# Optimization experiments

Hardware: AMD Instinct MI355X
Metric: run time of the kernel (lower is better)

Reference implementation:

```python
import jax, jax.numpy as jnp
import numpy as np

B, L, E, H = 4, 2048, 1024, 16
HD = E // H  # 64
ROPE_BASE = 10000.0


def setup_inputs() -> dict:
    key = jax.random.key(0)
    ks = jax.random.split(key, 4)
    x = jax.random.normal(ks[0], (B, L, E), dtype=jnp.float32)
    Wqkv = jax.random.normal(ks[1], (3 * E, E), dtype=jnp.float32) * (E ** -0.5)
    bqkv = jnp.zeros((3 * E,), dtype=jnp.float32)
    Wout = jax.random.normal(ks[2], (E, E), dtype=jnp.float32) * (E ** -0.5)
    bout = jnp.zeros((E,), dtype=jnp.float32)
    # RoPE tables: (1, 1, L, HD/2)
    half = HD // 2
    inv_freq = 1.0 / (ROPE_BASE ** (jnp.arange(half, dtype=jnp.float32) / half))
    t = jnp.arange(L, dtype=jnp.float32)
    freqs = t[:, None] * inv_freq[None, :]  # (L, half)
    cos = jnp.cos(freqs)[None, None]
    sin = jnp.sin(freqs)[None, None]
    return {"x": x, "cos": cos, "sin": sin, "Wqkv": Wqkv, "bqkv": bqkv,
            "Wout": Wout, "bout": bout}


def _apply_rope(q, k, cos, sin):
    half = q.shape[-1] // 2
    q1, q2 = q[..., :half], q[..., half:]
    k1, k2 = k[..., :half], k[..., half:]
    q_rot = jnp.concatenate([q1 * cos - q2 * sin, q1 * sin + q2 * cos], axis=-1)
    k_rot = jnp.concatenate([k1 * cos - k2 * sin, k1 * sin + k2 * cos], axis=-1)
    return q_rot, k_rot


def reference(x, cos, sin, Wqkv, bqkv, Wout, bout):
    b, l, e = x.shape
    qkv = x @ Wqkv.T + bqkv  # (B, L, 3E)
    q, k, v = jnp.split(qkv, 3, axis=-1)
    # (B, H, L, HD)
    q = q.reshape(b, l, H, HD).transpose(0, 2, 1, 3)
    k = k.reshape(b, l, H, HD).transpose(0, 2, 1, 3)
    v = v.reshape(b, l, H, HD).transpose(0, 2, 1, 3)
    q, k = _apply_rope(q, k, cos, sin)
    scale = 1.0 / jnp.sqrt(jnp.asarray(HD, dtype=x.dtype))
    scores = jnp.einsum('bhqd,bhkd->bhqk', q, k) * scale
    attn = jax.nn.softmax(scores, axis=-1)
    out = jnp.einsum('bhqk,bhkd->bhqd', attn, v)  # (B, H, L, HD)
    out = out.transpose(0, 2, 1, 3).reshape(b, l, e)
    out = out @ Wout.T + bout
    return out
```

## Files before the change

### kernel.cpp

```cpp
#include <hip/hip_runtime.h>
#include <math.h>

#define B 4
#define L 2048
#define E 1024
#define H 16
#define HD 64
#define MROWS (B*L)
#define E3 (3*E)

using bf16x8   = __attribute__((ext_vector_type(8))) short;
using f16x8    = __attribute__((ext_vector_type(8))) _Float16;
using floatx4  = __attribute__((ext_vector_type(4))) float;
using floatx16 = __attribute__((ext_vector_type(16))) float;

__device__ inline ushort f2bf(float x) {
    uint u = __float_as_uint(x);
    u += 0x7FFF + ((u >> 16) & 1);
    return (ushort)(u >> 16);
}
__device__ inline float bf2f(ushort h) { return __uint_as_float(((uint)h) << 16); }
__device__ inline ushort f2h(float x) { _Float16 h = (_Float16)x; return *(ushort*)&h; }

#if __has_builtin(__builtin_amdgcn_exp2f)
#define EXP2F(x) __builtin_amdgcn_exp2f(x)
#else
#define EXP2F(x) exp2f(x)
#endif

__device__ inline void async16(const void* g, void* l) {
    __builtin_amdgcn_global_load_lds(
        (const __attribute__((address_space(1))) uint*)g,
        (__attribute__((address_space(3))) uint*)l, 16, 0, 0);
}

__device__ inline uint pack_rtz(float odd, float even) {
    return __builtin_amdgcn_perm(__float_as_uint(odd), __float_as_uint(even), 0x07060302u);
}

#define N1Q ((size_t)MROWS * E / 4)
#define N2Q ((size_t)E3 * E / 4)
#define N3Q ((size_t)E * E / 4)
__global__ __launch_bounds__(256) void cvt_all(
        const float* __restrict__ x, const float* __restrict__ wq,
        const float* __restrict__ wo, ushort* __restrict__ x16,
        ushort* __restrict__ wq16, ushort* __restrict__ wo16)
{
    size_t i = (size_t)blockIdx.x * 256 + threadIdx.x;
    const float* src; ushort* dst; size_t j;
    if (i < N1Q)                  { src = x;  dst = x16;  j = i; }
    else if (i < N1Q + N2Q)       { src = wq; dst = wq16; j = i - N1Q; }
    else                          { src = wo; dst = wo16; j = i - N1Q - N2Q; }
    float4 v = ((const float4*)src)[j];
    ushort4 o;
    o.x = f2h(v.x); o.y = f2h(v.y); o.z = f2h(v.z); o.w = f2h(v.w);
    ((ushort4*)dst)[j] = o;
}

template<int MODE>
__global__ __launch_bounds__(256) void gemm_f16(
        const ushort* __restrict__ A16, const ushort* __restrict__ B16,
        const float* __restrict__ bias, float* __restrict__ Cf,
        ushort* __restrict__ qh, ushort* __restrict__ kh, ushort* __restrict__ vT,
        const float* __restrict__ cosT, const float* __restrict__ sinT,
        int Ndim, int Kdim)
{
    __shared__ ushort lds[2][8192];

    const int tid = threadIdx.x;
    const int w = tid >> 6, lane = tid & 63;
    const int g = lane >> 4, c = lane & 15;
    const int m0 = blockIdx.y * 128, n0 = blockIdx.x * 128;
    const int wm = w & 1, wn = w >> 1;

    const int rl0 = lane >> 2;
    const int jsw = (lane & 3) ^ ((lane >> 3) & 3);
    const ushort* gbase = (w < 2) ? A16 + (size_t)(m0 + 64 * (w & 1)) * Kdim
                                  : B16 + (size_t)(n0 + 64 * (w & 1)) * Kdim;
    const ushort* lanesrc = gbase + (size_t)rl0 * Kdim + jsw * 8;
    const int ldoff = (w >> 1) * 4096 + (w & 1) * 2048;

    floatx4 acc[4][4];
#pragma unroll
    for (int a = 0; a < 4; ++a)
#pragma unroll
        for (int bq = 0; bq < 4; ++bq) acc[a][bq] = (floatx4){0.f, 0.f, 0.f, 0.f};

    const int swz  = (g ^ ((c >> 1) & 3)) * 8;
    const int arow = wm * 2048 + c * 32;
    const int brow = 4096 + wn * 2048 + c * 32;

#pragma unroll
    for (int p = 0; p < 4; ++p)
        async16(lanesrc + (size_t)p * 16 * Kdim, &lds[0][ldoff + p * 512]);

    const int NK = Kdim >> 5;
    for (int kk = 0; kk < NK; ++kk) {
        const int pb = kk & 1;
        __syncthreads();

        if (kk + 1 < NK) {
            const ushort* ns = lanesrc + (size_t)(kk + 1) * 32;
#pragma unroll
            for (int p = 0; p < 4; ++p)
                async16(ns + (size_t)p * 16 * Kdim, &lds[pb ^ 1][ldoff + p * 512]);
        }

        const ushort* cur = &lds[pb][0];
        f16x8 af[4], bf[4];
#pragma unroll
        for (int t = 0; t < 4; ++t) {
            af[t] = *(const f16x8*)&cur[arow + t * 512 + swz];
            bf[t] = *(const f16x8*)&cur[brow + t * 512 + swz];
        }
#pragma unroll
        for (int mt = 0; mt < 4; ++mt)
#pragma unroll
            for (int nt = 0; nt < 4; ++nt)
                acc[mt][nt] = __builtin_amdgcn_mfma_f32_16x16x32_f16(af[mt], bf[nt], acc[mt][nt], 0, 0, 0);
    }

    const int colbase = n0 + wn * 64;
#pragma unroll
    for (int mt = 0; mt < 4; ++mt) {
        const int rowb = m0 + wm * 64 + mt * 16 + g * 4;
        if constexpr (MODE == 2) {
#pragma unroll
            for (int i = 0; i < 4; ++i) {
                const int row = rowb + i;
#pragma unroll
                for (int nt = 0; nt < 4; ++nt) {
                    const int col = colbase + nt * 16 + c;
                    Cf[(size_t)row * Ndim + col] = acc[mt][nt][i] + bias[col];
                }
            }
        } else {
            const int sec = colbase >> 10;
            const int hg  = (colbase & 1023) >> 6;
#pragma unroll
            for (int i = 0; i < 4; ++i) {
                const int row = rowb + i;
                const int bb = row >> 11;
                const int l  = row & (L - 1);
                if (sec < 2) {
                    ushort* dst = (sec == 0 ? qh : kh) + ((size_t)(bb * H + hg) * L + l) * HD;
                    const int sw = l & 7;
                    const float qs = (sec == 0) ? 0.18033688f : 1.0f;
#pragma unroll
                    for (int nt = 0; nt < 2; ++nt) {
                        const int d  = nt * 16 + c;
                        const int d2 = d + 32;
                        float v1 = acc[mt][nt][i]     + bias[colbase + d];
                        float v2 = acc[mt][nt + 2][i] + bias[colbase + d2];
                        float cs = cosT[l * 32 + d], sn = sinT[l * 32 + d];
                        dst[(((d  >> 3) ^ sw) << 3) | (d  & 7)] = f2bf((v1 * cs - v2 * sn) * qs);
                        dst[(((d2 >> 3) ^ sw) << 3) | (d2 & 7)] = f2bf((v1 * sn + v2 * cs) * qs);
                    }
                } else {
                    const int lp = (l & ~12) | ((l & 4) << 1) | ((l & 8) >> 1);
                    const int intile = ((((lp >> 3) & 7)) << 3);
#pragma unroll
                    for (int nt = 0; nt < 4; ++nt) {
                        const int d = nt * 16 + c;
                        float v = acc[mt][nt][i] + bias[colbase + d];
                        size_t idx = ((size_t)(bb * H + hg) * HD + d) * L
                                   + (l & ~63) + (intile ^ ((d & 7) << 3)) + (lp & 7);
                        vT[idx] = f2bf(v);
                    }
                }
            }
        }
    }
}

__global__ __launch_bounds__(256, 4) void flash_mfma4(
        const ushort* __restrict__ qh, const ushort* __restrict__ kh,
        const ushort* __restrict__ vT, ushort* __restrict__ attn16)
{
    __shared__ ushort Ks[2][4096];
    __shared__ ushort Vt[2][4096];

    const int tid  = threadIdx.x;
    const int w    = tid >> 6;
    const int lane = tid & 63;
    const int h    = lane >> 5;
    const int n    = lane & 31;
    const int b    = blockIdx.x >> 4;
    const int hd   = blockIdx.x & 15;
    const int q0   = blockIdx.y * 128;

    const ushort* khead = kh + (size_t)(b * H + hd) * L * HD;
    const ushort* vhead = vT + (size_t)(b * H + hd) * HD * L;

    const int q = q0 + 32 * w + n;
    const ushort* qrow = qh + ((size_t)(b * H + hd) * L + q) * HD;
    bf16x8 aq[4];
#pragma unroll
    for (int kd = 0; kd < 4; ++kd)
        aq[kd] = *(const bf16x8*)&qrow[((2 * kd + h) ^ (q & 7)) << 3];

    const int wk = w & 1;
    const ushort* ksrc = khead + (size_t)(32 * wk) * 64 + lane * 8;
    const ushort* vsrc = vhead + (size_t)(32 * wk + (lane >> 3)) * L + (lane & 7) * 8;

    const int NIT = L / 64;
    if (w < 2) {
#pragma unroll
        for (int p = 0; p < 4; ++p)
            async16(ksrc + p * 512, &Ks[0][32 * wk * 64 + p * 512]);
    } else {
#pragma unroll
        for (int p = 0; p < 4; ++p)
            async16(vsrc + (size_t)p * 8 * L, &Vt[0][32 * wk * 64 + p * 512]);
    }

    float l_i = 0.f;
    floatx16 o[2];
    o[0] = (floatx16)(0.f);
    o[1] = (floatx16)(0.f);

    for (int it = 0; it < NIT; ++it) {
        const int p = it & 1;
        __syncthreads();

        if (it + 1 < NIT) {
            if (w < 2) {
                const ushort* s = ksrc + (size_t)(it + 1) * 4096;
#pragma unroll
                for (int pp = 0; pp < 4; ++pp)
                    async16(s + pp * 512, &Ks[p ^ 1][32 * wk * 64 + pp * 512]);
            } else {
                const ushort* s = vsrc + (size_t)(it + 1) * 64;
#pragma unroll
                for (int pp = 0; pp < 4; ++pp)
                    async16(s + (size_t)pp * 8 * L, &Vt[p ^ 1][32 * wk * 64 + pp * 512]);
            }
        }

        const ushort* KsC = Ks[p];
        const ushort* VtC = Vt[p];

#pragma unroll
        for (int js = 0; js < 2; ++js) {
            floatx16 s = (floatx16)(-16.0f);
#pragma unroll
            for (int kd = 0; kd < 4; ++kd) {
                bf16x8 kf = *(const bf16x8*)&KsC[(32 * js + n) * 64 + (((2 * kd + h) ^ (n & 7)) << 3)];
                s = __builtin_amdgcn_mfma_f32_32x32x16_bf16(kf, aq[kd], s, 0, 0, 0);
            }

            float pv[16];
            float rs = 0.f;
#pragma unroll
            for (int rr = 0; rr < 4; ++rr) {
                float p0 = EXP2F(s[4 * rr + 0]);
                float p1 = EXP2F(s[4 * rr + 1]);
                float p2 = EXP2F(s[4 * rr + 2]);
                float p3 = EXP2F(s[4 * rr + 3]);
                pv[4 * rr + 0] = p0; pv[4 * rr + 1] = p1;
                pv[4 * rr + 2] = p2; pv[4 * rr + 3] = p3;
                rs += (p0 + p1) + (p2 + p3);
            }
            l_i += rs;

#pragma unroll
            for (int f = 0; f < 2; ++f) {
                uint bu[4];
                bu[0] = pack_rtz(pv[8 * f + 1], pv[8 * f + 0]);
                bu[1] = pack_rtz(pv[8 * f + 3], pv[8 * f + 2]);
                bu[2] = pack_rtz(pv[8 * f + 5], pv[8 * f + 4]);
                bu[3] = pack_rtz(pv[8 * f + 7], pv[8 * f + 6]);
                bf16x8 bp = *(const bf16x8*)&bu[0];
#pragma unroll
                for (int nt = 0; nt < 2; ++nt) {
                    bf16x8 vf = *(const bf16x8*)&VtC[(32 * nt + n) * 64 + (((4 * js + 2 * f + h) ^ (n & 7)) << 3)];
                    o[nt] = __builtin_amdgcn_mfma_f32_32x32x16_bf16(vf, bp, o[nt], 0, 0, 0);
                }
            }
        }
    }

    const float l_tot = l_i + __shfl_xor(l_i, 32, 64);
    const float inv = 1.f / l_tot;
    const size_t rowbase = ((size_t)(b * L + q)) * E + hd * HD;
#pragma unroll
    for (int nt = 0; nt < 2; ++nt)
#pragma unroll
        for (int rr = 0; rr < 4; ++rr) {
            const int d0 = 32 * nt + 8 * rr + 4 * h;
            ushort h0 = f2h(o[nt][4 * rr + 0] * inv);
            ushort h1 = f2h(o[nt][4 * rr + 1] * inv);
            ushort h2 = f2h(o[nt][4 * rr + 2] * inv);
            ushort h3 = f2h(o[nt][4 * rr + 3] * inv);
            uint2 hw;
            hw.x = (uint)h0 | ((uint)h1 << 16);
            hw.y = (uint)h2 | ((uint)h3 << 16);
            *(uint2*)&attn16[rowbase + d0] = hw;
        }
}

extern "C" void kernel_launch(void* const* d_in, const int* in_sizes, int n_in,
                              void* d_out, int out_size, void* d_ws, size_t ws_size,
                              hipStream_t stream) {
    const float* x    = (const float*)d_in[0];
    const float* cosT = (const float*)d_in[1];
    const float* sinT = (const float*)d_in[2];
    const float* Wqkv = (const float*)d_in[3];
    const float* bqkv = (const float*)d_in[4];
    const float* Wout = (const float*)d_in[5];
    const float* bout = (const float*)d_in[6];
    float* out = (float*)d_out;

    const size_t NX = (size_t)MROWS * E;
    ushort* us   = (ushort*)d_ws;
    ushort* qh   = us;
    ushort* kh   = us + NX;
    ushort* vTp  = us + 2 * NX;
    ushort* x16  = us + 3 * NX;
    ushort* at16 = us + 4 * NX;
    ushort* wq16 = us + 5 * NX;
    ushort* wo16 = wq16 + (size_t)E3 * E;

    const int cvt_blocks = (int)((N1Q + N2Q + N3Q + 255) / 256);
    cvt_all<<<cvt_blocks, 256, 0, stream>>>(x, Wqkv, Wout, x16, wq16, wo16);

    gemm_f16<1><<<dim3(E3 / 128, MROWS / 128), 256, 0, stream>>>(
        x16, wq16, bqkv, nullptr, qh, kh, vTp, cosT, sinT, E3, E);

    flash_mfma4<<<dim3(B * H, L / 128), 256, 0, stream>>>(qh, kh, vTp, at16);

    gemm_f16<2><<<dim3(E / 128, MROWS / 128), 256, 0, stream>>>(
        at16, wo16, bout, out, nullptr, nullptr, nullptr, nullptr, nullptr, E, E);
}
```

Measured before the change: 286.9 us.

## Rewrite GEMMs with 256-wide tiles, 4-stage async LDS pipeline, and swizzled block order

Replaces the 128x128 double-buffered GEMM with a 512-thread kernel using 256x256 (QKV) or 128x256 (out-proj) tiles. It uses a four-slot LDS ring with explicit vmcnt waits and a single barrier per K-step, plus MFMA priority boosting. Workgroup IDs are remapped in groups of 8 to improve L2 reuse. The goal is to raise MFMA density and overlap global loads with compute, at the cost of more LDS and registers per block, which lowers occupancy.

New measurement: 290.1 us. About the same (+1.1%).

```diff
diff --git a/kernel.cpp b/kernel.cpp
--- a/kernel.cpp
+++ b/kernel.cpp
@@ -37,6 +37,9 @@
 __device__ inline uint pack_rtz(float odd, float even) {
     return __builtin_amdgcn_perm(__float_as_uint(odd), __float_as_uint(even), 0x07060302u);
 }
+
+#define VMW(n) asm volatile("s_waitcnt vmcnt(" #n ")" ::: "memory")
+#define SBAR() asm volatile("s_barrier" ::: "memory")
 
 #define N1Q ((size_t)MROWS * E / 4)
 #define N2Q ((size_t)E3 * E / 4)
@@ -57,73 +60,108 @@
     ((ushort4*)dst)[j] = o;
 }
 
-template<int MODE>
-__global__ __launch_bounds__(256) void gemm_f16(
+template<int MODE, int MF>
+__global__ __launch_bounds__(512, 2) void gemm256(
         const ushort* __restrict__ A16, const ushort* __restrict__ B16,
         const float* __restrict__ bias, float* __restrict__ Cf,
         ushort* __restrict__ qh, ushort* __restrict__ kh, ushort* __restrict__ vT,
         const float* __restrict__ cosT, const float* __restrict__ sinT,
         int Ndim, int Kdim)
 {
-    __shared__ ushort lds[2][8192];
-
-    const int tid = threadIdx.x;
-    const int w = tid >> 6, lane = tid & 63;
-    const int g = lane >> 4, c = lane & 15;
-    const int m0 = blockIdx.y * 128, n0 = blockIdx.x * 128;
-    const int wm = w & 1, wn = w >> 1;
-
-    const int rl0 = lane >> 2;
-    const int jsw = (lane & 3) ^ ((lane >> 3) & 3);
-    const ushort* gbase = (w < 2) ? A16 + (size_t)(m0 + 64 * (w & 1)) * Kdim
-                                  : B16 + (size_t)(n0 + 64 * (w & 1)) * Kdim;
-    const ushort* lanesrc = gbase + (size_t)rl0 * Kdim + jsw * 8;
-    const int ldoff = (w >> 1) * 4096 + (w & 1) * 2048;
-
-    floatx4 acc[4][4];
-#pragma unroll
-    for (int a = 0; a < 4; ++a)
-#pragma unroll
-        for (int bq = 0; bq < 4; ++bq) acc[a][bq] = (floatx4){0.f, 0.f, 0.f, 0.f};
-
-    const int swz  = (g ^ ((c >> 1) & 3)) * 8;
-    const int arow = wm * 2048 + c * 32;
-    const int brow = 4096 + wn * 2048 + c * 32;
-
-#pragma unroll
-    for (int p = 0; p < 4; ++p)
-        async16(lanesrc + (size_t)p * 16 * Kdim, &lds[0][ldoff + p * 512]);
-
-    const int NK = Kdim >> 5;
-    for (int kk = 0; kk < NK; ++kk) {
-        const int pb = kk & 1;
-        __syncthreads();
-
-        if (kk + 1 < NK) {
-            const ushort* ns = lanesrc + (size_t)(kk + 1) * 32;
-#pragma unroll
-            for (int p = 0; p < 4; ++p)
-                async16(ns + (size_t)p * 16 * Kdim, &lds[pb ^ 1][ldoff + p * 512]);
-        }
-
-        const ushort* cur = &lds[pb][0];
-        f16x8 af[4], bf[4];
-#pragma unroll
-        for (int t = 0; t < 4; ++t) {
-            af[t] = *(const f16x8*)&cur[arow + t * 512 + swz];
-            bf[t] = *(const f16x8*)&cur[brow + t * 512 + swz];
-        }
-#pragma unroll
-        for (int mt = 0; mt < 4; ++mt)
-#pragma unroll
-            for (int nt = 0; nt < 4; ++nt)
-                acc[mt][nt] = __builtin_amdgcn_mfma_f32_16x16x32_f16(af[mt], bf[nt], acc[mt][nt], 0, 0, 0);
-    }
+    constexpr int BM    = MF * 32;
+    constexpr int ACOLS = MF * 1024;
+    constexpr int SLOT  = ACOLS + 8192;
+    constexpr int AP    = MF / 4;
+    __shared__ ushort lds[4][SLOT];
+
+    const int tid  = threadIdx.x;
+    const int w    = tid >> 6, lane = tid & 63;
+    const int g    = lane >> 4, c = lane & 15;
+    const int wm   = w >> 2,  wn = w & 3;
+
+    const int gx  = gridDim.x;
+    const int nwg = gx * gridDim.y;
+    int bid = blockIdx.y * gx + blockIdx.x;
+    bid = (bid & 7) * (nwg >> 3) + (bid >> 3);
+    const int m0 = (bid / gx) * BM;
+    const int n0 = (bid % gx) * 256;
+
+    const int rl = lane >> 2, q = lane & 3;
+    const ushort* srcA[AP]; int dstA[AP];
+#pragma unroll
+    for (int p = 0; p < AP; ++p) {
+        const int row = (w * AP + p) * 16 + rl;
+        const int kg  = q ^ ((row >> 1) & 3);
+        srcA[p] = A16 + (size_t)(m0 + row) * Kdim + kg * 8;
+        dstA[p] = (w * AP + p) * 512;
+    }
+    const ushort* srcB[2]; int dstB[2];
+#pragma unroll
+    for (int p = 0; p < 2; ++p) {
+        const int n  = (w * 2 + p) * 16 + rl;
+        const int kg = q ^ ((n >> 1) & 3);
+        srcB[p] = B16 + (size_t)(n0 + n) * Kdim + kg * 8;
+        dstB[p] = ACOLS + (w * 2 + p) * 512;
+    }
+
+    int scount = 0;
+    auto stage = [&]() {
+        ushort* base = &lds[scount & 3][0];
+#pragma unroll
+        for (int p = 0; p < AP; ++p) { async16(srcA[p], base + dstA[p]); srcA[p] += 32; }
+#pragma unroll
+        for (int p = 0; p < 2; ++p) { async16(srcB[p], base + dstB[p]); srcB[p] += 32; }
+        ++scount;
+    };
+
+    floatx4 acc[MF][4];
+#pragma unroll
+    for (int m = 0; m < MF; ++m)
+#pragma unroll
+        for (int n = 0; n < 4; ++n) acc[m][n] = (floatx4){0.f, 0.f, 0.f, 0.f};
+
+    const int swz   = (g ^ ((c >> 1) & 3)) << 3;
+    const int baseA = (wm * (MF * 16) + c) * 32 + swz;
+    const int baseB = ACOLS + (wn * 64 + c) * 32 + swz;
+
+    auto compute = [&](int sl) {
+        const ushort* cur = &lds[sl][0];
+        f16x8 af[MF], bf[4];
+#pragma unroll
+        for (int m = 0; m < MF; ++m) af[m] = *(const f16x8*)&cur[baseA + m * 512];
+#pragma unroll
+        for (int n = 0; n < 4; ++n)  bf[n] = *(const f16x8*)&cur[baseB + n * 512];
+        __builtin_amdgcn_s_setprio(1);
+#pragma unroll
+        for (int m = 0; m < MF; ++m)
+#pragma unroll
+            for (int n = 0; n < 4; ++n)
+                acc[m][n] = __builtin_amdgcn_mfma_f32_16x16x32_f16(af[m], bf[n], acc[m][n], 0, 0, 0);
+        __builtin_amdgcn_s_setprio(0);
+    };
+
+    const int NKH = Kdim >> 5;
+
+    stage();
+    stage();
+
+    for (int h = 0; h < NKH - 2; ++h) {
+        stage();
+        if constexpr (MF == 8) VMW(8); else VMW(6);
+        SBAR();
+        compute(h & 3);
+    }
+    if constexpr (MF == 8) VMW(4); else VMW(3);
+    SBAR();
+    compute((NKH - 2) & 3);
+    VMW(0);
+    SBAR();
+    compute((NKH - 1) & 3);
 
     const int colbase = n0 + wn * 64;
 #pragma unroll
-    for (int mt = 0; mt < 4; ++mt) {
-        const int rowb = m0 + wm * 64 + mt * 16 + g * 4;
+    for (int fm = 0; fm < MF; ++fm) {
+        const int rowb = m0 + wm * (MF * 16) + fm * 16 + g * 4;
         if constexpr (MODE == 2) {
 #pragma unroll
             for (int i = 0; i < 4; ++i) {
@@ -131,7 +169,7 @@
 #pragma unroll
                 for (int nt = 0; nt < 4; ++nt) {
                     const int col = colbase + nt * 16 + c;
-                    Cf[(size_t)row * Ndim + col] = acc[mt][nt][i] + bias[col];
+                    Cf[(size_t)row * Ndim + col] = acc[fm][nt][i] + bias[col];
                 }
             }
         } else {
@@ -150,8 +188,8 @@
                     for (int nt = 0; nt < 2; ++nt) {
                         const int d  = nt * 16 + c;
                         const int d2 = d + 32;
-                        float v1 = acc[mt][nt][i]     + bias[colbase + d];
-                        float v2 = acc[mt][nt + 2][i] + bias[colbase + d2];
+                        float v1 = acc[fm][nt][i]     + bias[colbase + d];
+                        float v2 = acc[fm][nt + 2][i] + bias[colbase + d2];
                         float cs = cosT[l * 32 + d], sn = sinT[l * 32 + d];
                         dst[(((d  >> 3) ^ sw) << 3) | (d  & 7)] = f2bf((v1 * cs - v2 * sn) * qs);
                         dst[(((d2 >> 3) ^ sw) << 3) | (d2 & 7)] = f2bf((v1 * sn + v2 * cs) * qs);
@@ -162,7 +200,7 @@
 #pragma unroll
                     for (int nt = 0; nt < 4; ++nt) {
                         const int d = nt * 16 + c;
-                        float v = acc[mt][nt][i] + bias[colbase + d];
+                        float v = acc[fm][nt][i] + bias[colbase + d];
                         size_t idx = ((size_t)(bb * H + hg) * HD + d) * L
                                    + (l & ~63) + (intile ^ ((d & 7) << 3)) + (lp & 7);
                         vT[idx] = f2bf(v);
@@ -324,11 +362,11 @@
     const int cvt_blocks = (int)((N1Q + N2Q + N3Q + 255) / 256);
     cvt_all<<<cvt_blocks, 256, 0, stream>>>(x, Wqkv, Wout, x16, wq16, wo16);
 
-    gemm_f16<1><<<dim3(E3 / 128, MROWS / 128), 256, 0, stream>>>(
+    gemm256<1, 8><<<dim3(E3 / 256, MROWS / 256), 512, 0, stream>>>(
         x16, wq16, bqkv, nullptr, qh, kh, vTp, cosT, sinT, E3, E);
 
     flash_mfma4<<<dim3(B * H, L / 128), 256, 0, stream>>>(qh, kh, vTp, at16);
 
-    gemm_f16<2><<<dim3(E / 128, MROWS / 128), 256, 0, stream>>>(
+    gemm256<2, 4><<<dim3(E / 256, MROWS / 128), 512, 0, stream>>>(
         at16, wo16, bout, out, nullptr, nullptr, nullptr, nullptr, nullptr, E, E);
 }
```
